# Kernel tuning notes

Hardware: AMD Instinct MI355X
Metric: run time of the kernel (lower is better)

## Reference

```python
import jax, jax.numpy as jnp
import numpy as np

HIDDEN = 2048
N_HEADS = 16
N_KV = 4
HEAD_DIM = 128
EPS = 1e-6
B = 8
L = 1024
PREFIX = 256
SUFFIX = L - PREFIX
N_COMPACT = PREFIX + B * SUFFIX  # 6400
T_FULL = B * L                   # 8192
ROPE_THETA = 10000.0


def _radix_indices():
    # full position (b, p) -> compact index
    scatter = np.empty(T_FULL, dtype=np.int64)
    for b in range(B):
        scatter[b * L: b * L + PREFIX] = np.arange(PREFIX)
        scatter[b * L + PREFIX: (b + 1) * L] = PREFIX + b * SUFFIX + np.arange(SUFFIX)
    # compact index -> first full occurrence
    fold = np.empty(N_COMPACT, dtype=np.int64)
    fold[:PREFIX] = np.arange(PREFIX)
    for b in range(B):
        fold[PREFIX + b * SUFFIX: PREFIX + (b + 1) * SUFFIX] = b * L + PREFIX + np.arange(SUFFIX)
    return scatter, fold


def setup_inputs() -> dict:
    key = jax.random.key(0)
    ks = jax.random.split(key, 8)
    scatter_np, fold_np = _radix_indices()
    # per-compact-token positions for RoPE
    pos = np.empty(N_COMPACT, dtype=np.float32)
    pos[:PREFIX] = np.arange(PREFIX)
    for b in range(B):
        pos[PREFIX + b * SUFFIX: PREFIX + (b + 1) * SUFFIX] = PREFIX + np.arange(SUFFIX)
    inv_freq = ROPE_THETA ** (-np.arange(HEAD_DIM // 2, dtype=np.float32) / (HEAD_DIM // 2))
    freqs = pos[:, None] * inv_freq[None, :]  # [N_c, 64]
    s = 0.02
    return {
        "hidden_states": jax.random.normal(ks[0], (N_COMPACT, HIDDEN), jnp.float32),
        "cos": jnp.asarray(np.cos(freqs), jnp.float32),
        "sin": jnp.asarray(np.sin(freqs), jnp.float32),
        "cu_seq_lengths": jnp.arange(B + 1, dtype=jnp.int32) * L,
        "max_seq_len": L,
        "fold_gather": jnp.asarray(fold_np),
        "scatter_indices": jnp.asarray(scatter_np),
        "wq": jax.random.normal(ks[1], (HIDDEN, N_HEADS * HEAD_DIM), jnp.float32) * s,
        "wk": jax.random.normal(ks[2], (HIDDEN, N_KV * HEAD_DIM), jnp.float32) * s,
        "wv": jax.random.normal(ks[3], (HIDDEN, N_KV * HEAD_DIM), jnp.float32) * s,
        "wo": jax.random.normal(ks[4], (N_HEADS * HEAD_DIM, HIDDEN), jnp.float32) * s,
        "q_norm_w": jnp.ones((HEAD_DIM,), jnp.float32),
        "k_norm_w": jnp.ones((HEAD_DIM,), jnp.float32),
    }


def _rmsnorm(x, w):
    xf = x.astype(jnp.float32)
    var = jnp.mean(xf * xf, axis=-1, keepdims=True)
    return (w * (xf * jax.lax.rsqrt(var + EPS))).astype(x.dtype)


def _rope(x, cos, sin):
    # x: [N, H, D]; cos/sin: [N, D/2]
    half = cos.shape[-1]
    x1, x2 = x[..., :half], x[..., half:2 * half]
    c, s = cos[:, None, :], sin[:, None, :]
    return jnp.concatenate([x1 * c - x2 * s, x1 * s + x2 * c], axis=-1)


def reference(hidden_states, cos, sin, cu_seq_lengths, max_seq_len,
              fold_gather, scatter_indices, wq, wk, wv, wo, q_norm_w, k_norm_w):
    N = hidden_states.shape[0]
    q = (hidden_states @ wq).reshape(N, N_HEADS, HEAD_DIM)
    k = (hidden_states @ wk).reshape(N, N_KV, HEAD_DIM)
    v = (hidden_states @ wv).reshape(N, N_KV, HEAD_DIM)
    q = _rope(_rmsnorm(q, q_norm_w), cos, sin)
    k = _rope(_rmsnorm(k, k_norm_w), cos, sin)
    # radix scatter: expand compact tokens to full varlen token stream
    qf = q[scatter_indices].reshape(B, L, N_HEADS, HEAD_DIM)
    kf = k[scatter_indices].reshape(B, L, N_KV, HEAD_DIM)
    vf = v[scatter_indices].reshape(B, L, N_KV, HEAD_DIM)
    group = N_HEADS // N_KV
    kf = jnp.repeat(kf, group, axis=2)
    vf = jnp.repeat(vf, group, axis=2)
    scale = HEAD_DIM ** -0.5
    scores = jnp.einsum('bqhd,bkhd->bhqk', qf, kf) * scale
    causal = jnp.tril(jnp.ones((L, L), dtype=bool))
    scores = jnp.where(causal[None, None], scores, jnp.finfo(scores.dtype).min)
    probs = jax.nn.softmax(scores, axis=-1)
    out = jnp.einsum('bhqk,bkhd->bqhd', probs, vf).reshape(T_FULL, N_HEADS * HEAD_DIM)
    # radix fold: gather back to compact tokens
    out_compact = out[fold_gather]
    return out_compact @ wo
```

## Files before the change

### kernel.cpp

```cpp
#include <hip/hip_runtime.h>
#include <hip/hip_bf16.h>

typedef __bf16 bf16;
typedef __bf16 bf16x4 __attribute__((ext_vector_type(4)));
typedef __bf16 bf16x8 __attribute__((ext_vector_type(8)));
typedef float f32x4 __attribute__((ext_vector_type(4)));

#define HID 2048
#define NHEADS 16
#define NKV 4
#define HD 128
#define NC 6400
#define KVW (NKV * HD)

__device__ __forceinline__ void async_cp16(const bf16* src, bf16* dst_lds) {
  __builtin_amdgcn_global_load_lds(
      (const __attribute__((address_space(1))) void*)src,
      (__attribute__((address_space(3))) void*)dst_lds, 16, 0, 0);
}

__device__ __forceinline__ void xcd_swizzle(int& bx, int& by) {
  int nx = gridDim.x;
  int nwg = nx * gridDim.y;
  int id = by * nx + bx;
  int q = nwg >> 3, r = nwg & 7;
  int xcd = id & 7, idx = id >> 3;
  int nid = (xcd < r ? xcd * (q + 1) : r * (q + 1) + (xcd - r) * q) + idx;
  bx = nid % nx;
  by = nid / nx;
}

__global__ __launch_bounds__(256) void k_cvt(const float* __restrict__ in,
                                             bf16* __restrict__ out) {
  size_t i = ((size_t)blockIdx.x * 256 + threadIdx.x) * 8;
  f32x4 a = *(const f32x4*)(in + i);
  f32x4 b = *(const f32x4*)(in + i + 4);
  bf16x8 t;
  for (int j = 0; j < 4; j++) {
    t[j] = (bf16)a[j];
    t[j + 4] = (bf16)b[j];
  }
  *(bf16x8*)(out + i) = t;
}

__global__ __launch_bounds__(256) void k_transpose(const float* __restrict__ in,
                                                   bf16* __restrict__ out,
                                                   int R, int C) {
  __shared__ bf16 tile[32][33];
  int bc = blockIdx.x * 32, br = blockIdx.y * 32;
  int tx = threadIdx.x & 31, ty = threadIdx.x >> 5;
  for (int i = 0; i < 32; i += 8)
    tile[ty + i][tx] = (bf16)in[(size_t)(br + ty + i) * C + bc + tx];
  __syncthreads();
  for (int i = 0; i < 32; i += 8)
    out[(size_t)(bc + ty + i) * R + br + tx] = tile[tx][ty + i];
}

__device__ __forceinline__ void gemm256_core(
    const bf16* __restrict__ A, const bf16* __restrict__ Bt, int m0, int nloc,
    int K, bf16* AsB, bf16* BsB, f32x4 (&acc)[2][4][4]) {
  const int tid = threadIdx.x;
  const int lane = tid & 63, wave = tid >> 6;
  const int l15 = lane & 15, quad = lane >> 4;
  const int wr = wave >> 2, wc = wave & 3;
  const int r0A = wr * 128 + l15;
  const int r0B = wc * 64 + l15;
  const int colOff0 = (quad * 8) ^ ((l15 & 7) << 3);
  const int colOff1 = (32 + quad * 8) ^ ((l15 & 7) << 3);
  const size_t offS0 =
      (size_t)(tid >> 3) * K + ((((tid & 7) ^ ((tid >> 3) & 7)) << 4) >> 1);
  const size_t offS1 = offS0 + (size_t)64 * K;
  const int dstW0 = wave * 512;
  const int dstW1 = 4096 + wave * 512;
  const bf16* Abase = A + (size_t)m0 * K;
  const bf16* Bbase = Bt + (size_t)nloc * K;
  const int KM = K - 1;

#define STAGE(gb, lds, dbuf, h, kc)                             \
  do {                                                          \
    const bf16* _s = (gb) + (size_t)(h) * 128 * K + (kc);       \
    bf16* _d = (lds) + (dbuf) * 16384 + (h) * 8192;             \
    async_cp16(_s + offS0, _d + dstW0);                         \
    async_cp16(_s + offS1, _d + dstW1);                         \
  } while (0)

#define LDA(dbuf, mh)                                           \
  do {                                                          \
    _Pragma("unroll") for (int i = 0; i < 4; i++) {             \
      int r = r0A + (mh) * 64 + i * 16;                         \
      const bf16* p = AsB + (dbuf) * 16384 + r * 64;            \
      a[i][0] = *(const bf16x8*)(p + colOff0);                  \
      a[i][1] = *(const bf16x8*)(p + colOff1);                  \
    }                                                           \
  } while (0)

#define LDB(dbuf, nh, bb)                                       \
  do {                                                          \
    _Pragma("unroll") for (int j = 0; j < 2; j++) {             \
      int r = r0B + (nh) * 32 + j * 16;                         \
      const bf16* p = BsB + (dbuf) * 16384 + r * 64;            \
      bb[j][0] = *(const bf16x8*)(p + colOff0);                 \
      bb[j][1] = *(const bf16x8*)(p + colOff1);                 \
    }                                                           \
  } while (0)

#define MFMAQ(mh, nh, bb)                                                    \
  do {                                                                       \
    __builtin_amdgcn_s_setprio(1);                                           \
    _Pragma("unroll") for (int i = 0; i < 4; i++)                            \
        _Pragma("unroll") for (int j = 0; j < 2; j++) {                      \
      acc[mh][i][(nh) * 2 + j] = __builtin_amdgcn_mfma_f32_16x16x32_bf16(    \
          a[i][0], bb[j][0], acc[mh][i][(nh) * 2 + j], 0, 0, 0);             \
      acc[mh][i][(nh) * 2 + j] = __builtin_amdgcn_mfma_f32_16x16x32_bf16(    \
          a[i][1], bb[j][1], acc[mh][i][(nh) * 2 + j], 0, 0, 0);             \
    }                                                                        \
    __builtin_amdgcn_s_setprio(0);                                           \
  } while (0)

  STAGE(Abase, AsB, 0, 0, 0);
  STAGE(Abase, AsB, 0, 1, 0);
  STAGE(Bbase, BsB, 0, 0, 0);
  STAGE(Bbase, BsB, 0, 1, 0);
  STAGE(Bbase, BsB, 1, 0, 64);
  STAGE(Bbase, BsB, 1, 1, 64);
  STAGE(Abase, AsB, 1, 0, 64);
  asm volatile("s_waitcnt vmcnt(6)" ::: "memory");
  __builtin_amdgcn_s_barrier();

  bf16x8 a[4][2], b0[2][2], b1[2][2];

  const int NIT = K >> 7;
#pragma unroll 1
  for (int it = 0; it < NIT; ++it) {
    const int kb = it << 7;
    LDA(0, 0);
    LDB(0, 0, b0);
    STAGE(Abase, AsB, 1, 1, (kb + 64) & KM);
    asm volatile("s_waitcnt lgkmcnt(8)");
    __builtin_amdgcn_s_barrier();
    asm volatile("s_waitcnt lgkmcnt(0)" ::: "memory");
    MFMAQ(0, 0, b0);
    __builtin_amdgcn_s_barrier();
    LDB(0, 1, b1);
    __builtin_amdgcn_s_barrier();
    asm volatile("s_waitcnt lgkmcnt(0)" ::: "memory");
    MFMAQ(0, 1, b1);
    __builtin_amdgcn_s_barrier();
    LDA(0, 1);
    STAGE(Bbase, BsB, 0, 0, (kb + 128) & KM);
    __builtin_amdgcn_s_barrier();
    asm volatile("s_waitcnt lgkmcnt(0)" ::: "memory");
    MFMAQ(1, 0, b0);
    __builtin_amdgcn_s_barrier();
    STAGE(Bbase, BsB, 0, 1, (kb + 128) & KM);
    __builtin_amdgcn_s_barrier();
    asm volatile("s_waitcnt lgkmcnt(0)" ::: "memory");
    MFMAQ(1, 1, b1);
    asm volatile("s_waitcnt vmcnt(4)" ::: "memory");
    __builtin_amdgcn_s_barrier();
    LDA(1, 0);
    LDB(1, 0, b0);
    STAGE(Abase, AsB, 0, 0, (kb + 128) & KM);
    asm volatile("s_waitcnt lgkmcnt(8)");
    __builtin_amdgcn_s_barrier();
    asm volatile("s_waitcnt lgkmcnt(0)" ::: "memory");
    MFMAQ(0, 0, b0);
    __builtin_amdgcn_s_barrier();
    LDB(1, 1, b1);
    STAGE(Abase, AsB, 0, 1, (kb + 128) & KM);
    __builtin_amdgcn_s_barrier();
    asm volatile("s_waitcnt lgkmcnt(0)" ::: "memory");
    MFMAQ(0, 1, b1);
    __builtin_amdgcn_s_barrier();
    LDA(1, 1);
    STAGE(Bbase, BsB, 1, 0, (kb + 192) & KM);
    __builtin_amdgcn_s_barrier();
    asm volatile("s_waitcnt lgkmcnt(0)" ::: "memory");
    MFMAQ(1, 0, b0);
    __builtin_amdgcn_s_barrier();
    STAGE(Bbase, BsB, 1, 1, (kb + 192) & KM);
    STAGE(Abase, AsB, 1, 0, (kb + 192) & KM);
    __builtin_amdgcn_s_barrier();
    asm volatile("s_waitcnt lgkmcnt(0)" ::: "memory");
    MFMAQ(1, 1, b1);
    asm volatile("s_waitcnt vmcnt(6)" ::: "memory");
    __builtin_amdgcn_s_barrier();
  }
#undef STAGE
#undef LDA
#undef LDB
#undef MFMAQ
}

__global__ __launch_bounds__(512, 2) void k_proj(const bf16* __restrict__ A,
                                                 const bf16* __restrict__ wqT,
                                                 const bf16* __restrict__ wkT,
                                                 const bf16* __restrict__ wvT,
                                                 bf16* __restrict__ qb,
                                                 bf16* __restrict__ kb,
                                                 bf16* __restrict__ vtb) {
  __shared__ __align__(16) bf16 smem[2][2][256][64];
  int bx = blockIdx.x, by = blockIdx.y;
  xcd_swizzle(bx, by);
  int n0 = bx * 256, m0 = by * 256;

  const bf16* bt;
  int nloc, outsel;
  if (n0 < HID) {
    bt = wqT; nloc = n0; outsel = 0;
  } else if (n0 < HID + KVW) {
    bt = wkT; nloc = n0 - HID; outsel = 1;
  } else {
    bt = wvT; nloc = n0 - HID - KVW; outsel = 2;
  }

  const f32x4 fz = {0.0f, 0.0f, 0.0f, 0.0f};
  f32x4 acc[2][4][4];
#pragma unroll
  for (int mh = 0; mh < 2; mh++)
#pragma unroll
    for (int i = 0; i < 4; i++)
#pragma unroll
      for (int j = 0; j < 4; j++) acc[mh][i][j] = fz;

  gemm256_core(A, bt, m0, nloc, HID, &smem[0][0][0][0], &smem[1][0][0][0], acc);

  int tid = threadIdx.x, lane = tid & 63, wave = tid >> 6;
  int l15 = lane & 15, quad = lane >> 4;
  int wr = wave >> 2, wc = wave & 3;

  if (outsel == 2) {
    asm volatile("s_waitcnt vmcnt(0)" ::: "memory");
    __syncthreads();
    bf16* sm = &smem[0][0][0][0];
#pragma unroll
    for (int mh = 0; mh < 2; mh++)
#pragma unroll
      for (int i = 0; i < 4; i++)
#pragma unroll
        for (int nj = 0; nj < 4; nj++) {
          int col = wc * 64 + nj * 16 + l15;
          int row = wr * 128 + mh * 64 + i * 16 + quad * 4;
          int idx = col * 256 + ((row + ((col & 7) << 3)) & 255);
          bf16x4 v4 = {(bf16)acc[mh][i][nj][0], (bf16)acc[mh][i][nj][1],
                       (bf16)acc[mh][i][nj][2], (bf16)acc[mh][i][nj][3]};
          *(bf16x4*)&sm[idx] = v4;
        }
    __syncthreads();
#pragma unroll
    for (int p = 0; p < 4; p++) {
      int cc = p * 64 + (tid >> 3);
      int h = tid & 7;
#pragma unroll
      for (int j = 0; j < 4; j++) {
        int row8 = h * 32 + j * 8;
        bf16x8 v =
            *(const bf16x8*)&sm[cc * 256 + ((row8 + ((cc & 7) << 3)) & 255)];
        *(bf16x8*)(vtb + (size_t)(nloc + cc) * NC + m0 + row8) = v;
      }
    }
  } else {
#pragma unroll
    for (int mh = 0; mh < 2; mh++)
#pragma unroll
      for (int i = 0; i < 4; i++)
#pragma unroll
        for (int nj = 0; nj < 4; nj++)
#pragma unroll
          for (int r = 0; r < 4; r++) {
            int row = m0 + wr * 128 + mh * 64 + i * 16 + quad * 4 + r;
            int col = nloc + wc * 64 + nj * 16 + l15;
            float v = acc[mh][i][nj][r];
            if (outsel == 0)
              qb[(size_t)row * HID + col] = (bf16)v;
            else
              kb[(size_t)row * KVW + col] = (bf16)v;
          }
  }
}

__global__ __launch_bounds__(512, 2) void k_gemm_out(const bf16* __restrict__ A,
                                                     const bf16* __restrict__ Bt,
                                                     float* __restrict__ C,
                                                     int M, int N, int K) {
  __shared__ __align__(16) bf16 smem[2][2][256][64];
  int bx = blockIdx.x, by = blockIdx.y;
  xcd_swizzle(bx, by);
  int n0 = bx * 256, m0 = by * 256;

  const f32x4 fz = {0.0f, 0.0f, 0.0f, 0.0f};
  f32x4 acc[2][4][4];
#pragma unroll
  for (int mh = 0; mh < 2; mh++)
#pragma unroll
    for (int i = 0; i < 4; i++)
#pragma unroll
      for (int j = 0; j < 4; j++) acc[mh][i][j] = fz;

  gemm256_core(A, Bt, m0, n0, K, &smem[0][0][0][0], &smem[1][0][0][0], acc);

  int tid = threadIdx.x, lane = tid & 63, wave = tid >> 6;
  int l15 = lane & 15, quad = lane >> 4;
  int wr = wave >> 2, wc = wave & 3;
#pragma unroll
  for (int mh = 0; mh < 2; mh++)
#pragma unroll
    for (int i = 0; i < 4; i++)
#pragma unroll
      for (int nj = 0; nj < 4; nj++)
#pragma unroll
        for (int r = 0; r < 4; r++) {
          int row = m0 + wr * 128 + mh * 64 + i * 16 + quad * 4 + r;
          int col = n0 + wc * 64 + nj * 16 + l15;
          C[(size_t)row * N + col] = acc[mh][i][nj][r];
        }
}

__global__ __launch_bounds__(256) void k_normrope(bf16* __restrict__ q,
                                                  bf16* __restrict__ k,
                                                  const float* __restrict__ cs,
                                                  const float* __restrict__ sn,
                                                  const float* __restrict__ qw,
                                                  const float* __restrict__ kw) {
  int pair = blockIdx.x * 4 + (threadIdx.x >> 6);
  int lane = threadIdx.x & 63;
  int n = pair / 20, hh = pair % 20;
  bf16* base;
  const float* w;
  if (hh < 16) {
    base = q + (size_t)n * HID + hh * HD;
    w = qw;
  } else {
    base = k + (size_t)n * KVW + (hh - 16) * HD;
    w = kw;
  }
  float x1 = (float)base[lane], x2 = (float)base[lane + 64];
  float ss = x1 * x1 + x2 * x2;
  for (int o = 32; o; o >>= 1) ss += __shfl_xor(ss, o);
  float inv = rsqrtf(ss * (1.0f / 128.0f) + 1e-6f);
  float x1n = x1 * inv * w[lane];
  float x2n = x2 * inv * w[lane + 64];
  float c = cs[(size_t)n * 64 + lane];
  float s = sn[(size_t)n * 64 + lane];
  base[lane] = (bf16)(x1n * c - x2n * s);
  base[lane + 64] = (bf16)(x1n * s + x2n * c);
}

__global__ __launch_bounds__(256) void k_attn(const bf16* __restrict__ qb,
                                              const bf16* __restrict__ kb,
                                              const bf16* __restrict__ vt,
                                              bf16* __restrict__ ob) {
  int qt = blockIdx.x;
  int h = blockIdx.y;
  int kh = h >> 2;
  int tid = threadIdx.x;
  int lane = tid & 63, wave = tid >> 6;
  int l15 = lane & 15, quad = lane >> 4;

  int b, p0, nbase;
  if (qt < 4) {
    b = 0;
    p0 = qt * 64;
    nbase = qt * 64;
  } else {
    int t = qt - 4;
    b = t / 12;
    int ti = t - b * 12;
    p0 = 256 + ti * 64;
    nbase = 256 + b * 768 + ti * 64;
  }

  __shared__ __align__(16) bf16 Ks[64][136];
  __shared__ __align__(16) bf16 Vs[128][72];
  __shared__ __align__(16) bf16 Ps[4][16][72];

  bf16x8 aq[4];
  {
    const bf16* qp =
        qb + (size_t)(nbase + wave * 16 + l15) * HID + h * HD + quad * 8;
    for (int ks = 0; ks < 4; ks++) aq[ks] = *(const bf16x8*)(qp + ks * 32);
  }
  int qpos[4];
  for (int r = 0; r < 4; r++) qpos[r] = p0 + wave * 16 + quad * 4 + r;

  const f32x4 fz = {0.0f, 0.0f, 0.0f, 0.0f};
  f32x4 oacc[8];
  for (int i = 0; i < 8; i++) oacc[i] = fz;
  float mrow[4], lrow[4];
  for (int r = 0; r < 4; r++) {
    mrow[r] = -3.0e38f;
    lrow[r] = 0.0f;
  }
  const float scale = 0.08838834764831845f;

  int nkt = p0 / 64 + 1;
  for (int kt = 0; kt < nkt; kt++) {
    int kpos0 = kt * 64;
    int kbase = (kpos0 < 256) ? kpos0 : 256 + b * 768 + (kpos0 - 256);
    __syncthreads();
    for (int s = 0; s < 4; s++) {
      int c = tid + 256 * s;
      int key = c >> 4, dc = c & 15;
      *(uint4*)&Ks[key][dc * 8] =
          *(const uint4*)(kb + (size_t)(kbase + key) * KVW + kh * HD + dc * 8);
    }
    for (int s = 0; s < 4; s++) {
      int c = tid + 256 * s;
      int d = c >> 3, kc = c & 7;
      *(uint4*)&Vs[d][kc * 8] =
          *(const uint4*)(vt + (size_t)(kh * HD + d) * NC + kbase + kc * 8);
    }
    __syncthreads();

    bool diag = (kt == nkt - 1);
    float sv[4][4];
    for (int nt = 0; nt < 4; nt++) {
      f32x4 z = fz;
      for (int ks = 0; ks < 4; ks++) {
        bf16x8 kf = *(const bf16x8*)&Ks[nt * 16 + l15][ks * 32 + quad * 8];
        z = __builtin_amdgcn_mfma_f32_16x16x32_bf16(aq[ks], kf, z, 0, 0, 0);
      }
      int kpos = kpos0 + nt * 16 + l15;
      for (int r = 0; r < 4; r++) {
        float v = z[r] * scale;
        if (diag && kpos > qpos[r]) v = -1.0e30f;
        sv[nt][r] = v;
      }
    }
    float alpha[4];
    for (int r = 0; r < 4; r++) {
      float mx = fmaxf(fmaxf(sv[0][r], sv[1][r]), fmaxf(sv[2][r], sv[3][r]));
      for (int o = 1; o < 16; o <<= 1) mx = fmaxf(mx, __shfl_xor(mx, o));
      float mnew = fmaxf(mrow[r], mx);
      alpha[r] = __expf(mrow[r] - mnew);
      mrow[r] = mnew;
      float ps = 0.0f;
      for (int nt = 0; nt < 4; nt++) {
        float p = __expf(sv[nt][r] - mnew);
        sv[nt][r] = p;
        ps += p;
      }
      for (int o = 1; o < 16; o <<= 1) ps += __shfl_xor(ps, o);
      lrow[r] = lrow[r] * alpha[r] + ps;
    }
    for (int i = 0; i < 8; i++)
      for (int r = 0; r < 4; r++) oacc[i][r] *= alpha[r];

    for (int nt = 0; nt < 4; nt++)
      for (int r = 0; r < 4; r++)
        Ps[wave][quad * 4 + r][nt * 16 + l15] = (bf16)sv[nt][r];
    __syncthreads();
    bf16x8 pa[2];
    for (int ks = 0; ks < 2; ks++)
      pa[ks] = *(const bf16x8*)&Ps[wave][l15][ks * 32 + quad * 8];
    for (int dt = 0; dt < 8; dt++)
      for (int ks = 0; ks < 2; ks++) {
        bf16x8 vf = *(const bf16x8*)&Vs[dt * 16 + l15][ks * 32 + quad * 8];
        oacc[dt] =
            __builtin_amdgcn_mfma_f32_16x16x32_bf16(pa[ks], vf, oacc[dt], 0, 0, 0);
      }
  }
  for (int r = 0; r < 4; r++) {
    float il = 1.0f / lrow[r];
    bf16* op = ob + (size_t)(nbase + wave * 16 + quad * 4 + r) * HID + h * HD;
    for (int dt = 0; dt < 8; dt++) op[dt * 16 + l15] = (bf16)(oacc[dt][r] * il);
  }
}

extern "C" void kernel_launch(void* const* d_in, const int* in_sizes, int n_in,
                              void* d_out, int out_size, void* d_ws,
                              size_t ws_size, hipStream_t stream) {
  const float* hs = (const float*)d_in[0];
  const float* cs = (const float*)d_in[1];
  const float* sn = (const float*)d_in[2];
  const float* wq = (const float*)d_in[7];
  const float* wk = (const float*)d_in[8];
  const float* wv = (const float*)d_in[9];
  const float* wo = (const float*)d_in[10];
  const float* qnw = (const float*)d_in[11];
  const float* knw = (const float*)d_in[12];
  float* out = (float*)d_out;

  bf16* hsb = (bf16*)d_out;
  bf16* wqT = hsb + (size_t)NC * HID;
  bf16* wkT = wqT + (size_t)HID * HID;
  bf16* wvT = wkT + (size_t)KVW * HID;
  bf16* qb  = (bf16*)d_in[0];
  bf16* ab  = qb + (size_t)NC * HID;
  bf16* woT = qb;
  bf16* kb  = (bf16*)d_ws;
  bf16* vtb = kb + (size_t)NC * KVW;

  k_cvt<<<dim3(NC * HID / (256 * 8)), 256, 0, stream>>>(hs, hsb);
  k_transpose<<<dim3(HID / 32, HID / 32), 256, 0, stream>>>(wq, wqT, HID, HID);
  k_transpose<<<dim3(KVW / 32, HID / 32), 256, 0, stream>>>(wk, wkT, HID, KVW);
  k_transpose<<<dim3(KVW / 32, HID / 32), 256, 0, stream>>>(wv, wvT, HID, KVW);

  k_proj<<<dim3((HID + 2 * KVW) / 256, NC / 256), 512, 0, stream>>>(
      hsb, wqT, wkT, wvT, qb, kb, vtb);

  k_normrope<<<dim3(NC * 20 / 4), 256, 0, stream>>>(qb, kb, cs, sn, qnw, knw);

  k_attn<<<dim3(100, NHEADS), 256, 0, stream>>>(qb, kb, vtb, ab);

  k_transpose<<<dim3(HID / 32, HID / 32), 256, 0, stream>>>(wo, woT, HID, HID);

  k_gemm_out<<<dim3(HID / 256, NC / 256), 512, 0, stream>>>(ab, woT, out, NC, HID, HID);
}
```

Baseline: 472.2 us.

## Prefetch next K/V tile into registers and schedule longest attention tiles first

The attention kernel now loads the next K/V tile from global memory into registers while the current tile's MFMAs run, then writes it to LDS behind a barrier. This hides global load latency and removes one block-wide sync per iteration, replacing it with a per-wave lgkmcnt wait for the P tile. Query tiles are reordered so that the longest causal tiles (latest positions, interleaved across batches) launch first, which should even out tail imbalance. s_setprio hints are also added around the MFMA sections. The cost is higher register pressure from the prefetch buffers, which may lower occupancy.

```diff
diff --git a/kernel.cpp b/kernel.cpp
--- a/kernel.cpp
+++ b/kernel.cpp
@@ -350,7 +350,7 @@
                                               const bf16* __restrict__ kb,
                                               const bf16* __restrict__ vt,
                                               bf16* __restrict__ ob) {
-  int qt = blockIdx.x;
+  int t = blockIdx.x;
   int h = blockIdx.y;
   int kh = h >> 2;
   int tid = threadIdx.x;
@@ -358,35 +358,54 @@
   int l15 = lane & 15, quad = lane >> 4;
 
   int b, p0, nbase;
-  if (qt < 4) {
-    b = 0;
-    p0 = qt * 64;
-    nbase = qt * 64;
-  } else {
-    int t = qt - 4;
-    b = t / 12;
-    int ti = t - b * 12;
+  if (t < 96) {
+    int ti = 11 - (t >> 3);
+    b = t & 7;
     p0 = 256 + ti * 64;
     nbase = 256 + b * 768 + ti * 64;
+  } else {
+    int pt = 99 - t;
+    b = 0;
+    p0 = pt * 64;
+    nbase = pt * 64;
   }
 
   __shared__ __align__(16) bf16 Ks[64][136];
   __shared__ __align__(16) bf16 Vs[128][72];
   __shared__ __align__(16) bf16 Ps[4][16][72];
+
+  const bf16* kpt[4];
+  const bf16* vpt[4];
+  bf16* kds[4];
+  bf16* vds[4];
+#pragma unroll
+  for (int s = 0; s < 4; s++) {
+    int c = tid + 256 * s;
+    int key = c >> 4, dc = c & 15;
+    kpt[s] = kb + (size_t)key * KVW + kh * HD + dc * 8;
+    kds[s] = &Ks[key][dc * 8];
+    int d = c >> 3, kc = c & 7;
+    vpt[s] = vt + (size_t)(kh * HD + d) * NC + kc * 8;
+    vds[s] = &Vs[d][kc * 8];
+  }
 
   bf16x8 aq[4];
   {
     const bf16* qp =
         qb + (size_t)(nbase + wave * 16 + l15) * HID + h * HD + quad * 8;
+#pragma unroll
     for (int ks = 0; ks < 4; ks++) aq[ks] = *(const bf16x8*)(qp + ks * 32);
   }
   int qpos[4];
+#pragma unroll
   for (int r = 0; r < 4; r++) qpos[r] = p0 + wave * 16 + quad * 4 + r;
 
   const f32x4 fz = {0.0f, 0.0f, 0.0f, 0.0f};
   f32x4 oacc[8];
+#pragma unroll
   for (int i = 0; i < 8; i++) oacc[i] = fz;
   float mrow[4], lrow[4];
+#pragma unroll
   for (int r = 0; r < 4; r++) {
     mrow[r] = -3.0e38f;
     lrow[r] = 0.0f;
@@ -394,33 +413,47 @@
   const float scale = 0.08838834764831845f;
 
   int nkt = p0 / 64 + 1;
+
+  uint4 kreg[4], vreg[4];
+#pragma unroll
+  for (int s = 0; s < 4; s++) kreg[s] = *(const uint4*)kpt[s];
+#pragma unroll
+  for (int s = 0; s < 4; s++) vreg[s] = *(const uint4*)vpt[s];
+#pragma unroll
+  for (int s = 0; s < 4; s++) *(uint4*)kds[s] = kreg[s];
+#pragma unroll
+  for (int s = 0; s < 4; s++) *(uint4*)vds[s] = vreg[s];
+  __syncthreads();
+
   for (int kt = 0; kt < nkt; kt++) {
     int kpos0 = kt * 64;
-    int kbase = (kpos0 < 256) ? kpos0 : 256 + b * 768 + (kpos0 - 256);
-    __syncthreads();
-    for (int s = 0; s < 4; s++) {
-      int c = tid + 256 * s;
-      int key = c >> 4, dc = c & 15;
-      *(uint4*)&Ks[key][dc * 8] =
-          *(const uint4*)(kb + (size_t)(kbase + key) * KVW + kh * HD + dc * 8);
+    bool hasnext = (kt + 1 < nkt);
+    if (hasnext) {
+      int kposN = kpos0 + 64;
+      int kbaseN = (kposN < 256) ? kposN : 256 + b * 768 + (kposN - 256);
+#pragma unroll
+      for (int s = 0; s < 4; s++)
+        kreg[s] = *(const uint4*)(kpt[s] + (size_t)kbaseN * KVW);
+#pragma unroll
+      for (int s = 0; s < 4; s++)
+        vreg[s] = *(const uint4*)(vpt[s] + kbaseN);
+      __builtin_amdgcn_sched_barrier(0);
     }
-    for (int s = 0; s < 4; s++) {
-      int c = tid + 256 * s;
-      int d = c >> 3, kc = c & 7;
-      *(uint4*)&Vs[d][kc * 8] =
-          *(const uint4*)(vt + (size_t)(kh * HD + d) * NC + kbase + kc * 8);
-    }
-    __syncthreads();
 
     bool diag = (kt == nkt - 1);
     float sv[4][4];
+#pragma unroll
     for (int nt = 0; nt < 4; nt++) {
       f32x4 z = fz;
+      __builtin_amdgcn_s_setprio(1);
+#pragma unroll
       for (int ks = 0; ks < 4; ks++) {
         bf16x8 kf = *(const bf16x8*)&Ks[nt * 16 + l15][ks * 32 + quad * 8];
         z = __builtin_amdgcn_mfma_f32_16x16x32_bf16(aq[ks], kf, z, 0, 0, 0);
       }
+      __builtin_amdgcn_s_setprio(0);
       int kpos = kpos0 + nt * 16 + l15;
+#pragma unroll
       for (int r = 0; r < 4; r++) {
         float v = z[r] * scale;
         if (diag && kpos > qpos[r]) v = -1.0e30f;
@@ -428,6 +461,7 @@
       }
     }
     float alpha[4];
+#pragma unroll
     for (int r = 0; r < 4; r++) {
       float mx = fmaxf(fmaxf(sv[0][r], sv[1][r]), fmaxf(sv[2][r], sv[3][r]));
       for (int o = 1; o < 16; o <<= 1) mx = fmaxf(mx, __shfl_xor(mx, o));
@@ -435,6 +469,7 @@
       alpha[r] = __expf(mrow[r] - mnew);
       mrow[r] = mnew;
       float ps = 0.0f;
+#pragma unroll
       for (int nt = 0; nt < 4; nt++) {
         float p = __expf(sv[nt][r] - mnew);
         sv[nt][r] = p;
@@ -443,26 +478,46 @@
       for (int o = 1; o < 16; o <<= 1) ps += __shfl_xor(ps, o);
       lrow[r] = lrow[r] * alpha[r] + ps;
     }
+#pragma unroll
     for (int i = 0; i < 8; i++)
+#pragma unroll
       for (int r = 0; r < 4; r++) oacc[i][r] *= alpha[r];
 
+#pragma unroll
     for (int nt = 0; nt < 4; nt++)
+#pragma unroll
       for (int r = 0; r < 4; r++)
         Ps[wave][quad * 4 + r][nt * 16 + l15] = (bf16)sv[nt][r];
-    __syncthreads();
+    asm volatile("s_waitcnt lgkmcnt(0)" ::: "memory");
     bf16x8 pa[2];
+#pragma unroll
     for (int ks = 0; ks < 2; ks++)
       pa[ks] = *(const bf16x8*)&Ps[wave][l15][ks * 32 + quad * 8];
+    __builtin_amdgcn_s_setprio(1);
+#pragma unroll
     for (int dt = 0; dt < 8; dt++)
+#pragma unroll
       for (int ks = 0; ks < 2; ks++) {
         bf16x8 vf = *(const bf16x8*)&Vs[dt * 16 + l15][ks * 32 + quad * 8];
         oacc[dt] =
             __builtin_amdgcn_mfma_f32_16x16x32_bf16(pa[ks], vf, oacc[dt], 0, 0, 0);
       }
-  }
+    __builtin_amdgcn_s_setprio(0);
+
+    if (hasnext) {
+      __syncthreads();
+#pragma unroll
+      for (int s = 0; s < 4; s++) *(uint4*)kds[s] = kreg[s];
+#pragma unroll
+      for (int s = 0; s < 4; s++) *(uint4*)vds[s] = vreg[s];
+      __syncthreads();
+    }
+  }
+#pragma unroll
   for (int r = 0; r < 4; r++) {
     float il = 1.0f / lrow[r];
     bf16* op = ob + (size_t)(nbase + wave * 16 + quad * 4 + r) * HID + h * HD;
+#pragma unroll
     for (int dt = 0; dt < 8; dt++) op[dt * 16 + l15] = (bf16)(oacc[dt][r] * il);
   }
 }
```

Result: slower. 541.6 us (+14.7%).
